# Optimization experiments

Hardware: AMD Instinct MI355X
Metric: run time of the kernel (lower is better)

## Reference

```python
import jax, jax.numpy as jnp
import numpy as np

B, T, D, R = 16, 4096, 512, 256

def setup_inputs() -> dict:
    key = jax.random.key(0)
    z = jax.random.normal(key, (B, T, D), dtype=jnp.float32)
    # init values from the module: gegenbauer_weights = [3,0,0], temporal_alpha = -10.0
    gegenbauer_weights = jnp.array([3.0, 0.0, 0.0], dtype=jnp.float32)
    temporal_alpha = jnp.array(-10.0, dtype=jnp.float32)
    # uniformly spaced landmarks, truncated to int like torch.linspace(...).long()
    landmarks = jnp.asarray(np.linspace(0, T - 1, R).astype(np.int64))
    return {"z": z, "gegenbauer_weights": gegenbauer_weights, "temporal_alpha": temporal_alpha, "landmarks": landmarks}

def reference(z, gegenbauer_weights, temporal_alpha, landmarks):
    Bz, Tz, d = z.shape
    # F.normalize(z, dim=-1) with eps=1e-12
    norm = jnp.linalg.norm(z, axis=-1, keepdims=True)
    Q = z / jnp.maximum(norm, 1e-12)
    K = Q[:, landmarks, :]                                   # [B, R, d]
    C = jnp.einsum('btd,brd->btr', Q, K)                     # [B, T, R]
    positions = jnp.arange(Tz)[:, None]                      # [T, 1]
    lm = landmarks[None, :]                                  # [1, R]
    causal_mask = (lm < positions).astype(z.dtype)           # [T, R]
    C_masked = C * causal_mask[None, :, :]
    # Gegenbauer mixture
    alpha = jax.nn.softmax(gegenbauer_weights)
    P1 = (1.0 + C_masked) * 0.5
    P2 = (3.0 * C_masked * C_masked - 1.0) * 0.5
    P3 = (5.0 * C_masked * C_masked * C_masked - 3.0 * C_masked) * 0.5
    Phi = alpha[0] * P1 + alpha[1] * P2 + alpha[2] * P3
    # temporal decay
    temporal_dist = jnp.clip((positions.astype(z.dtype) - lm.astype(z.dtype)) / Tz, 0.0, None)  # [T, R]
    alpha_td = jax.nn.softplus(temporal_alpha)
    Phi = Phi * jnp.exp(-alpha_td * temporal_dist)[None, :, :]
    # rowsum normalize
    row_sum = jnp.maximum(Phi.sum(axis=-1, keepdims=True), 1e-6)
    Phi = Phi / row_sum
    # append constant-1 basis column
    ones = jnp.ones((Bz, Tz, 1), dtype=z.dtype)
    return jnp.concatenate([Phi, ones], axis=-1)             # [B, T, R+1]
```

## Files before the change

kernel.cpp:

```cpp
#include <hip/hip_runtime.h>


typedef float f32x4 __attribute__((ext_vector_type(4)));
typedef short s16x8 __attribute__((ext_vector_type(8)));
typedef unsigned short u16x4 __attribute__((ext_vector_type(4)));
typedef unsigned short u16x8 __attribute__((ext_vector_type(8)));

__device__ __forceinline__ unsigned short f2bf(float f) {
    unsigned u = __builtin_bit_cast(unsigned, f);
    return (unsigned short)((u + 0x7FFFu + ((u >> 16) & 1u)) >> 16);
}

__device__ __forceinline__ int load_lm(const void* lms_raw, int idx) {
    const int* l32 = (const int*)lms_raw;
    if (l32[1] == 0) {
        const long long* l64 = (const long long*)lms_raw;
        return (int)l64[idx];
    }
    return l32[idx];
}

__device__ __forceinline__ void scalars(const float* gw, const float* ta,
                                        float& a0, float& a1, float& a2, float& atd) {
    float w0 = gw[0], w1 = gw[1], w2 = gw[2];
    float wm = fmaxf(w0, fmaxf(w1, w2));
    float e0 = __expf(w0 - wm), e1 = __expf(w1 - wm), e2 = __expf(w2 - wm);
    float einv = 1.0f / (e0 + e1 + e2);
    a0 = e0 * einv; a1 = e1 * einv; a2 = e2 * einv;
    float tv = ta[0];
    atd = (tv > 0.0f) ? (tv + log1pf(__expf(-tv))) : log1pf(__expf(tv));
}

__global__ void build_kt(const float* __restrict__ z,
                         const void* __restrict__ lms_raw,
                         unsigned char* __restrict__ kb) {
    const int b = blockIdx.x >> 8;
    const int r = blockIdx.x & 255;
    const int L = threadIdx.x;
    const int lm = load_lm(lms_raw, r);

    const f32x4* zrow = (const f32x4*)(z + ((size_t)b * 4096 + (size_t)lm) * 512);
    f32x4 v0 = zrow[L * 2 + 0];
    f32x4 v1 = zrow[L * 2 + 1];
    float ss = v0.x*v0.x + v0.y*v0.y + v0.z*v0.z + v0.w*v0.w
             + v1.x*v1.x + v1.y*v1.y + v1.z*v1.z + v1.w*v1.w;
    #pragma unroll
    for (int off = 32; off >= 1; off >>= 1) ss += __shfl_xor(ss, off, 64);
    float inv = 1.0f / fmaxf(sqrtf(ss), 1e-12f);

    u16x8 o;
    o[0]=f2bf(v0.x*inv); o[1]=f2bf(v0.y*inv); o[2]=f2bf(v0.z*inv); o[3]=f2bf(v0.w*inv);
    o[4]=f2bf(v1.x*inv); o[5]=f2bf(v1.y*inv); o[6]=f2bf(v1.z*inv); o[7]=f2bf(v1.w*inv);

    const int rt = r >> 4;
    const int c  = r & 15;
    const int ks = L >> 2;
    const int g  = L & 3;
    size_t off = (size_t)b * 262144
               + (size_t)(ks * 16 + rt) * 1024 + (size_t)(c * 4 + g) * 16;
    *(u16x8*)(kb + off) = o;
}

#define LDB(S, KS) do { \
    B##S##0 = *(const u16x8*)(kbw + (size_t)((KS) * 16 + rt0 + 0) * 1024); \
    B##S##1 = *(const u16x8*)(kbw + (size_t)((KS) * 16 + rt0 + 1) * 1024); \
} while (0)

#define LDA(AV, KK) do { \
    AV##0 = *(const s16x8*)(qtile + ((KK) * 2 + 0) * 1024 + aoff); \
    AV##1 = *(const s16x8*)(qtile + ((KK) * 2 + 1) * 1024 + aoff); \
} while (0)

#define MM(AV, S) do { \
    s16x8 ba_ = __builtin_bit_cast(s16x8, B##S##0); \
    s16x8 bb_ = __builtin_bit_cast(s16x8, B##S##1); \
    acc00 = __builtin_amdgcn_mfma_f32_16x16x32_bf16(AV##0, ba_, acc00, 0, 0, 0); \
    acc01 = __builtin_amdgcn_mfma_f32_16x16x32_bf16(AV##0, bb_, acc01, 0, 0, 0); \
    acc10 = __builtin_amdgcn_mfma_f32_16x16x32_bf16(AV##1, ba_, acc10, 0, 0, 0); \
    acc11 = __builtin_amdgcn_mfma_f32_16x16x32_bf16(AV##1, bb_, acc11, 0, 0, 0); \
} while (0)

#define STEP(KS, AC, AN, S) do { \
    if ((KS) + 1 < 16) LDA(AN, (KS) + 1); \
    MM(AC, S); \
    if ((KS) + 4 < 16) LDB(S, (KS) + 4); \
} while (0)

__global__ __launch_bounds__(512, 6) void nystrom_mfma(const float* __restrict__ z,
                                                       const float* __restrict__ gw,
                                                       const float* __restrict__ ta,
                                                       const void* __restrict__ lms_raw,
                                                       const unsigned char* __restrict__ kb,
                                                       float* __restrict__ out) {
    __shared__ unsigned char qtile[32 * 1024];
    __shared__ float s_invn[32];
    __shared__ float s_rs[8][32];
    __shared__ float s_rsi[32];

    const int tid  = threadIdx.x;
    const int lane = tid & 63;
    const int w    = tid >> 6;

    const int wgid = (blockIdx.x & 7) * 256 + (blockIdx.x >> 3);
    const int b    = wgid >> 7;
    const int t0   = (wgid & 127) * 32;

    const int c = lane & 15;
    const int g = lane >> 4;
    const int aoff = (c * 4 + g) * 16;

    float sa0, sa1, sa2, alpha_td;
    scalars(gw, ta, sa0, sa1, sa2, alpha_td);
    const float C0 = 0.5f * (sa0 - sa1);

    const unsigned char* kbw = kb + (size_t)b * 262144 + (size_t)(c * 4 + g) * 16;
    const int rt0 = 2 * w;

    u16x8 B00, B01, B10, B11, B20, B21, B30, B31;
    LDB(0, 0); LDB(1, 1); LDB(2, 2); LDB(3, 3);

    const int lmv0 = load_lm(lms_raw, 32 * w + c);
    const int lmv1 = load_lm(lms_raw, 32 * w + 16 + c);
    const float elm0 = __expf(alpha_td * (float)lmv0 * (1.0f / 4096.0f));
    const float elm1 = __expf(alpha_td * (float)lmv1 * (1.0f / 4096.0f));

    {
        const int row = tid >> 4, part = tid & 15;
        const f32x4* zr = (const f32x4*)(z + ((size_t)b * 4096 + (size_t)(t0 + row)) * 512);
        f32x4 v[8];
        #pragma unroll
        for (int i = 0; i < 8; ++i) v[i] = zr[part + 16 * i];
        const int base = (row >> 4) * 1024 + ((row & 15) * 4 + ((part >> 1) & 3)) * 16
                       + (part & 1) * 8 + (part >> 3) * 2048;
        float ss = 0.0f;
        #pragma unroll
        for (int i = 0; i < 8; ++i) {
            f32x4 vv = v[i];
            ss += vv.x*vv.x + vv.y*vv.y + vv.z*vv.z + vv.w*vv.w;
            u16x4 hh; hh[0]=f2bf(vv.x); hh[1]=f2bf(vv.y); hh[2]=f2bf(vv.z); hh[3]=f2bf(vv.w);
            *(u16x4*)(qtile + base + i * 4096) = hh;
        }
        ss += __shfl_xor(ss, 1, 64);
        ss += __shfl_xor(ss, 2, 64);
        ss += __shfl_xor(ss, 4, 64);
        ss += __shfl_xor(ss, 8, 64);
        if (part == 0) s_invn[row] = 1.0f / fmaxf(sqrtf(ss), 1e-12f);
    }
    __syncthreads();

    f32x4 acc00 = {0,0,0,0}, acc01 = {0,0,0,0};
    f32x4 acc10 = {0,0,0,0}, acc11 = {0,0,0,0};

    s16x8 A00, A01, A10, A11;
    LDA(A0, 0);

    STEP( 0, A0, A1, 0);  STEP( 1, A1, A0, 1);
    STEP( 2, A0, A1, 2);  STEP( 3, A1, A0, 3);
    STEP( 4, A0, A1, 0);  STEP( 5, A1, A0, 1);
    STEP( 6, A0, A1, 2);  STEP( 7, A1, A0, 3);
    STEP( 8, A0, A1, 0);  STEP( 9, A1, A0, 1);
    STEP(10, A0, A1, 2);  STEP(11, A1, A0, 3);
    STEP(12, A0, A1, 0);  STEP(13, A1, A0, 1);
    STEP(14, A0, A1, 2);  STEP(15, A1, A0, 3);

    f32x4 acc[2][2] = {{acc00, acc01}, {acc10, acc11}};
    const int   lmv[2] = {lmv0, lmv1};
    const float elm[2] = {elm0, elm1};

    float eA[2], eB[4];
    #pragma unroll
    for (int tf = 0; tf < 2; ++tf)
        eA[tf] = __expf(-alpha_td * (float)(t0 + tf * 16) * (1.0f / 4096.0f));
    #pragma unroll
    for (int q = 0; q < 4; ++q)
        eB[q] = __expf(-alpha_td * (float)(g * 4 + q) * (1.0f / 4096.0f));
    float invn[2][4];
    #pragma unroll
    for (int tf = 0; tf < 2; ++tf)
        #pragma unroll
        for (int q = 0; q < 4; ++q)
            invn[tf][q] = s_invn[tf * 16 + g * 4 + q];

    float phi[2][2][4];
    float rsum[2][4];
    #pragma unroll
    for (int tf = 0; tf < 2; ++tf) {
        #pragma unroll
        for (int q = 0; q < 4; ++q) {
            int tg = t0 + tf * 16 + g * 4 + q;
            float et = eA[tf] * eB[q];
            float s = 0.0f;
            #pragma unroll
            for (int nf = 0; nf < 2; ++nf) {
                float v = acc[tf][nf][q] * invn[tf][q];
                float p;
                if (lmv[nf] < tg) {
                    float c2 = v * v;
                    float p1 = fmaf(0.5f, v, 0.5f);
                    float p2 = fmaf(1.5f, c2, -0.5f);
                    float p3 = v * fmaf(2.5f, c2, -1.5f);
                    p = (sa0 * p1 + sa1 * p2 + sa2 * p3) * (et * elm[nf]);
                } else {
                    p = C0;
                }
                phi[tf][nf][q] = p;
                s += p;
            }
            rsum[tf][q] = s;
        }
    }

    #pragma unroll
    for (int tf = 0; tf < 2; ++tf)
        #pragma unroll
        for (int q = 0; q < 4; ++q) {
            float s = rsum[tf][q];
            s += __shfl_xor(s, 1, 64);
            s += __shfl_xor(s, 2, 64);
            s += __shfl_xor(s, 4, 64);
            s += __shfl_xor(s, 8, 64);
            rsum[tf][q] = s;
        }
    if (c == 0) {
        #pragma unroll
        for (int tf = 0; tf < 2; ++tf)
            #pragma unroll
            for (int q = 0; q < 4; ++q)
                s_rs[w][tf * 16 + g * 4 + q] = rsum[tf][q];
    }
    __syncthreads();
    if (tid < 32) {
        float s = 0.0f;
        #pragma unroll
        for (int i = 0; i < 8; ++i) s += s_rs[i][tid];
        s_rsi[tid] = 1.0f / fmaxf(s, 1e-6f);
    }
    __syncthreads();

    #pragma unroll
    for (int tf = 0; tf < 2; ++tf)
        #pragma unroll
        for (int q = 0; q < 4; ++q) {
            int tl = tf * 16 + g * 4 + q;
            float ri = s_rsi[tl];
            size_t obase = ((size_t)b * 4096 + (size_t)(t0 + tl)) * 257
                         + (size_t)(32 * w + c);
            #pragma unroll
            for (int nf = 0; nf < 2; ++nf)
                out[obase + nf * 16] = phi[tf][nf][q] * ri;
        }
    if (tid < 32)
        out[((size_t)b * 4096 + (size_t)(t0 + tid)) * 257 + 256] = 1.0f;
}

extern "C" void kernel_launch(void* const* d_in, const int* in_sizes, int n_in,
                              void* d_out, int out_size, void* d_ws, size_t ws_size,
                              hipStream_t stream) {
    const float* z   = (const float*)d_in[0];
    const float* gw  = (const float*)d_in[1];
    const float* ta  = (const float*)d_in[2];
    const void*  lms = (const void*)d_in[3];
    float* out = (float*)d_out;
    unsigned char* kb = (unsigned char*)d_ws;

    build_kt<<<16 * 256, 64, 0, stream>>>(z, lms, kb);
    nystrom_mfma<<<2048, 512, 0, stream>>>(z, gw, ta, lms, kb, out);
}
```

Before: 66.46 us.

## Precompute bf16 Q in MFMA-packed layout in separate prep kernel

Adds a prep kernel that converts z to bf16 in the MFMA operand layout and stores per-row inverse norms in workspace. The main kernel then streams A operands straight from global memory with a 4-deep register prefetch instead of staging them in LDS behind a barrier. This removes the LDS tile and the __syncthreads from the main kernel, but adds an extra full pass over z plus a write and re-read of the bf16 copy. The occupancy hint in the launch bounds also drops from 6 to 4.

```diff
diff --git a/kernel.cpp b/kernel.cpp
--- a/kernel.cpp
+++ b/kernel.cpp
@@ -3,7 +3,6 @@
 
 typedef float f32x4 __attribute__((ext_vector_type(4)));
 typedef short s16x8 __attribute__((ext_vector_type(8)));
-typedef unsigned short u16x4 __attribute__((ext_vector_type(4)));
 typedef unsigned short u16x8 __attribute__((ext_vector_type(8)));
 
 __device__ __forceinline__ unsigned short f2bf(float f) {
@@ -31,6 +30,31 @@
     atd = (tv > 0.0f) ? (tv + log1pf(__expf(-tv))) : log1pf(__expf(tv));
 }
 
+__global__ __launch_bounds__(256) void prep_q(const float* __restrict__ z,
+                                              unsigned char* __restrict__ qp,
+                                              float* __restrict__ invn) {
+    const int gw   = blockIdx.x * 4 + (threadIdx.x >> 6);
+    const int lane = threadIdx.x & 63;
+
+    const f32x4* zr = (const f32x4*)(z + (size_t)gw * 512);
+    f32x4 v0 = zr[lane * 2 + 0];
+    f32x4 v1 = zr[lane * 2 + 1];
+    float ss = v0.x*v0.x + v0.y*v0.y + v0.z*v0.z + v0.w*v0.w
+             + v1.x*v1.x + v1.y*v1.y + v1.z*v1.z + v1.w*v1.w;
+    #pragma unroll
+    for (int off = 32; off >= 1; off >>= 1) ss += __shfl_xor(ss, off, 64);
+    if (lane == 0) invn[gw] = 1.0f / fmaxf(sqrtf(ss), 1e-12f);
+
+    u16x8 o;
+    o[0]=f2bf(v0.x); o[1]=f2bf(v0.y); o[2]=f2bf(v0.z); o[3]=f2bf(v0.w);
+    o[4]=f2bf(v1.x); o[5]=f2bf(v1.y); o[6]=f2bf(v1.z); o[7]=f2bf(v1.w);
+
+    size_t addr = (size_t)(gw >> 5) * 32768
+                + (size_t)(((lane >> 2) * 2 + ((gw >> 4) & 1)) * 1024)
+                + (size_t)((((lane & 3) * 16 + (gw & 15)) * 16));
+    *(u16x8*)(qp + addr) = o;
+}
+
 __global__ void build_kt(const float* __restrict__ z,
                          const void* __restrict__ lms_raw,
                          unsigned char* __restrict__ kb) {
@@ -66,34 +90,32 @@
     B##S##1 = *(const u16x8*)(kbw + (size_t)((KS) * 16 + rt0 + 1) * 1024); \
 } while (0)
 
-#define LDA(AV, KK) do { \
-    AV##0 = *(const s16x8*)(qtile + ((KK) * 2 + 0) * 1024 + aoff); \
-    AV##1 = *(const s16x8*)(qtile + ((KK) * 2 + 1) * 1024 + aoff); \
-} while (0)
-
-#define MM(AV, S) do { \
+#define LDA(S, KS) do { \
+    A##S##0 = *(const s16x8*)(qpb + ((KS) * 2 + 0) * 1024); \
+    A##S##1 = *(const s16x8*)(qpb + ((KS) * 2 + 1) * 1024); \
+} while (0)
+
+#define MM(S) do { \
     s16x8 ba_ = __builtin_bit_cast(s16x8, B##S##0); \
     s16x8 bb_ = __builtin_bit_cast(s16x8, B##S##1); \
-    acc00 = __builtin_amdgcn_mfma_f32_16x16x32_bf16(AV##0, ba_, acc00, 0, 0, 0); \
-    acc01 = __builtin_amdgcn_mfma_f32_16x16x32_bf16(AV##0, bb_, acc01, 0, 0, 0); \
-    acc10 = __builtin_amdgcn_mfma_f32_16x16x32_bf16(AV##1, ba_, acc10, 0, 0, 0); \
-    acc11 = __builtin_amdgcn_mfma_f32_16x16x32_bf16(AV##1, bb_, acc11, 0, 0, 0); \
-} while (0)
-
-#define STEP(KS, AC, AN, S) do { \
-    if ((KS) + 1 < 16) LDA(AN, (KS) + 1); \
-    MM(AC, S); \
-    if ((KS) + 4 < 16) LDB(S, (KS) + 4); \
-} while (0)
-
-__global__ __launch_bounds__(512, 6) void nystrom_mfma(const float* __restrict__ z,
-                                                       const float* __restrict__ gw,
+    acc00 = __builtin_amdgcn_mfma_f32_16x16x32_bf16(A##S##0, ba_, acc00, 0, 0, 0); \
+    acc01 = __builtin_amdgcn_mfma_f32_16x16x32_bf16(A##S##0, bb_, acc01, 0, 0, 0); \
+    acc10 = __builtin_amdgcn_mfma_f32_16x16x32_bf16(A##S##1, ba_, acc10, 0, 0, 0); \
+    acc11 = __builtin_amdgcn_mfma_f32_16x16x32_bf16(A##S##1, bb_, acc11, 0, 0, 0); \
+} while (0)
+
+#define STEP(KS, S) do { \
+    MM(S); \
+    if ((KS) + 4 < 16) { LDA(S, (KS) + 4); LDB(S, (KS) + 4); } \
+} while (0)
+
+__global__ __launch_bounds__(512, 4) void nystrom_mfma(const float* __restrict__ gw,
                                                        const float* __restrict__ ta,
                                                        const void* __restrict__ lms_raw,
+                                                       const unsigned char* __restrict__ qp,
                                                        const unsigned char* __restrict__ kb,
+                                                       const float* __restrict__ invng,
                                                        float* __restrict__ out) {
-    __shared__ unsigned char qtile[32 * 1024];
-    __shared__ float s_invn[32];
     __shared__ float s_rs[8][32];
     __shared__ float s_rsi[32];
 
@@ -103,65 +125,39 @@
 
     const int wgid = (blockIdx.x & 7) * 256 + (blockIdx.x >> 3);
     const int b    = wgid >> 7;
-    const int t0   = (wgid & 127) * 32;
+    const int tt   = wgid & 127;
+    const int t0   = tt * 32;
 
     const int c = lane & 15;
     const int g = lane >> 4;
-    const int aoff = (c * 4 + g) * 16;
 
     float sa0, sa1, sa2, alpha_td;
     scalars(gw, ta, sa0, sa1, sa2, alpha_td);
     const float C0 = 0.5f * (sa0 - sa1);
 
+    const unsigned char* qpb = qp + (size_t)(b * 128 + tt) * 32768 + (size_t)lane * 16;
     const unsigned char* kbw = kb + (size_t)b * 262144 + (size_t)(c * 4 + g) * 16;
     const int rt0 = 2 * w;
 
     u16x8 B00, B01, B10, B11, B20, B21, B30, B31;
-    LDB(0, 0); LDB(1, 1); LDB(2, 2); LDB(3, 3);
+    s16x8 A00, A01, A10, A11, A20, A21, A30, A31;
+    LDA(0, 0); LDB(0, 0);
+    LDA(1, 1); LDB(1, 1);
+    LDA(2, 2); LDB(2, 2);
+    LDA(3, 3); LDB(3, 3);
 
     const int lmv0 = load_lm(lms_raw, 32 * w + c);
     const int lmv1 = load_lm(lms_raw, 32 * w + 16 + c);
     const float elm0 = __expf(alpha_td * (float)lmv0 * (1.0f / 4096.0f));
     const float elm1 = __expf(alpha_td * (float)lmv1 * (1.0f / 4096.0f));
 
-    {
-        const int row = tid >> 4, part = tid & 15;
-        const f32x4* zr = (const f32x4*)(z + ((size_t)b * 4096 + (size_t)(t0 + row)) * 512);
-        f32x4 v[8];
-        #pragma unroll
-        for (int i = 0; i < 8; ++i) v[i] = zr[part + 16 * i];
-        const int base = (row >> 4) * 1024 + ((row & 15) * 4 + ((part >> 1) & 3)) * 16
-                       + (part & 1) * 8 + (part >> 3) * 2048;
-        float ss = 0.0f;
-        #pragma unroll
-        for (int i = 0; i < 8; ++i) {
-            f32x4 vv = v[i];
-            ss += vv.x*vv.x + vv.y*vv.y + vv.z*vv.z + vv.w*vv.w;
-            u16x4 hh; hh[0]=f2bf(vv.x); hh[1]=f2bf(vv.y); hh[2]=f2bf(vv.z); hh[3]=f2bf(vv.w);
-            *(u16x4*)(qtile + base + i * 4096) = hh;
-        }
-        ss += __shfl_xor(ss, 1, 64);
-        ss += __shfl_xor(ss, 2, 64);
-        ss += __shfl_xor(ss, 4, 64);
-        ss += __shfl_xor(ss, 8, 64);
-        if (part == 0) s_invn[row] = 1.0f / fmaxf(sqrtf(ss), 1e-12f);
-    }
-    __syncthreads();
-
     f32x4 acc00 = {0,0,0,0}, acc01 = {0,0,0,0};
     f32x4 acc10 = {0,0,0,0}, acc11 = {0,0,0,0};
 
-    s16x8 A00, A01, A10, A11;
-    LDA(A0, 0);
-
-    STEP( 0, A0, A1, 0);  STEP( 1, A1, A0, 1);
-    STEP( 2, A0, A1, 2);  STEP( 3, A1, A0, 3);
-    STEP( 4, A0, A1, 0);  STEP( 5, A1, A0, 1);
-    STEP( 6, A0, A1, 2);  STEP( 7, A1, A0, 3);
-    STEP( 8, A0, A1, 0);  STEP( 9, A1, A0, 1);
-    STEP(10, A0, A1, 2);  STEP(11, A1, A0, 3);
-    STEP(12, A0, A1, 0);  STEP(13, A1, A0, 1);
-    STEP(14, A0, A1, 2);  STEP(15, A1, A0, 3);
+    STEP( 0, 0);  STEP( 1, 1);  STEP( 2, 2);  STEP( 3, 3);
+    STEP( 4, 0);  STEP( 5, 1);  STEP( 6, 2);  STEP( 7, 3);
+    STEP( 8, 0);  STEP( 9, 1);  STEP(10, 2);  STEP(11, 3);
+    STEP(12, 0);  STEP(13, 1);  STEP(14, 2);  STEP(15, 3);
 
     f32x4 acc[2][2] = {{acc00, acc01}, {acc10, acc11}};
     const int   lmv[2] = {lmv0, lmv1};
@@ -179,7 +175,7 @@
     for (int tf = 0; tf < 2; ++tf)
         #pragma unroll
         for (int q = 0; q < 4; ++q)
-            invn[tf][q] = s_invn[tf * 16 + g * 4 + q];
+            invn[tf][q] = invng[b * 4096 + t0 + tf * 16 + g * 4 + q];
 
     float phi[2][2][4];
     float rsum[2][4];
@@ -261,8 +257,12 @@
     const float* ta  = (const float*)d_in[2];
     const void*  lms = (const void*)d_in[3];
     float* out = (float*)d_out;
-    unsigned char* kb = (unsigned char*)d_ws;
-
+
+    unsigned char* qp   = (unsigned char*)d_ws;
+    unsigned char* kb   = qp + (size_t)16 * 128 * 32 * 1024;
+    float*         invn = (float*)(kb + (size_t)16 * 262144);
+
+    prep_q<<<16384, 256, 0, stream>>>(z, qp, invn);
     build_kt<<<16 * 256, 64, 0, stream>>>(z, lms, kb);
-    nystrom_mfma<<<2048, 512, 0, stream>>>(z, gw, ta, lms, kb, out);
-}
+    nystrom_mfma<<<2048, 512, 0, stream>>>(gw, ta, lms, qp, kb, invn, out);
+}
```

After: 109.0 us. 1.64x slower.

## Make MFMA blocks persistent over four row tiles with prefetched z loads

Applied to the files above, without the earlier changes.

Each workgroup now handles 128 time steps in four 32-row iterations instead of one, and the grid shrinks from 2048 to 512 blocks. The next tile's z rows are loaded into registers while the current tile's MFMA runs, and the K fragments are reloaded after each GEMM. The LDS Q tile moves to a row-major layout with an XOR swizzle to avoid bank conflicts. The aim is to hide global-load latency and cut per-block setup, at the cost of more registers (launch bounds lowered to 4 waves) and fewer blocks to spread over the CUs.

```diff
diff --git a/kernel.cpp b/kernel.cpp
--- a/kernel.cpp
+++ b/kernel.cpp
@@ -67,8 +67,9 @@
 } while (0)
 
 #define LDA(AV, KK) do { \
-    AV##0 = *(const s16x8*)(qtile + ((KK) * 2 + 0) * 1024 + aoff); \
-    AV##1 = *(const s16x8*)(qtile + ((KK) * 2 + 1) * 1024 + aoff); \
+    int kw_ = ((KK) * 64 + g * 16) ^ swz; \
+    AV##0 = *(const s16x8*)(qtile + (c     ) * 1024 + kw_); \
+    AV##1 = *(const s16x8*)(qtile + (c + 16) * 1024 + kw_); \
 } while (0)
 
 #define MM(AV, S) do { \
@@ -86,28 +87,44 @@
     if ((KS) + 4 < 16) LDB(S, (KS) + 4); \
 } while (0)
 
-__global__ __launch_bounds__(512, 6) void nystrom_mfma(const float* __restrict__ z,
+#define LDV(J) do { \
+    const f32x4* zr_ = (const f32x4*)(z + ((size_t)b * 4096 \
+                        + (size_t)(tbase + (J) * 32 + row)) * 512); \
+    V0 = zr_[part +  0]; V1 = zr_[part + 16]; \
+    V2 = zr_[part + 32]; V3 = zr_[part + 48]; \
+    V4 = zr_[part + 64]; V5 = zr_[part + 80]; \
+    V6 = zr_[part + 96]; V7 = zr_[part + 112]; \
+} while (0)
+
+#define STV(I, VV) do { \
+    ss += VV.x*VV.x + VV.y*VV.y + VV.z*VV.z + VV.w*VV.w; \
+    u16x4 hh_; hh_[0]=f2bf(VV.x); hh_[1]=f2bf(VV.y); hh_[2]=f2bf(VV.z); hh_[3]=f2bf(VV.w); \
+    int wi_ = ((part + 16 * (I)) * 8) ^ ((row & 7) << 4); \
+    *(u16x4*)(qtile + row * 1024 + wi_) = hh_; \
+} while (0)
+
+__global__ __launch_bounds__(512, 4) void nystrom_mfma(const float* __restrict__ z,
                                                        const float* __restrict__ gw,
                                                        const float* __restrict__ ta,
                                                        const void* __restrict__ lms_raw,
                                                        const unsigned char* __restrict__ kb,
                                                        float* __restrict__ out) {
     __shared__ unsigned char qtile[32 * 1024];
-    __shared__ float s_invn[32];
+    __shared__ float s_aux[2][32];
     __shared__ float s_rs[8][32];
-    __shared__ float s_rsi[32];
 
     const int tid  = threadIdx.x;
     const int lane = tid & 63;
     const int w    = tid >> 6;
 
-    const int wgid = (blockIdx.x & 7) * 256 + (blockIdx.x >> 3);
-    const int b    = wgid >> 7;
-    const int t0   = (wgid & 127) * 32;
+    const int wgid  = (blockIdx.x & 7) * 64 + (blockIdx.x >> 3);
+    const int b     = wgid >> 5;
+    const int tbase = (wgid & 31) * 128;
 
     const int c = lane & 15;
     const int g = lane >> 4;
-    const int aoff = (c * 4 + g) * 16;
+    const int row = tid >> 4, part = tid & 15;
+    const int swz = (c & 7) << 4;
 
     float sa0, sa1, sa2, alpha_td;
     scalars(gw, ta, sa0, sa1, sa2, alpha_td);
@@ -115,142 +132,141 @@
 
     const unsigned char* kbw = kb + (size_t)b * 262144 + (size_t)(c * 4 + g) * 16;
     const int rt0 = 2 * w;
-
-    u16x8 B00, B01, B10, B11, B20, B21, B30, B31;
-    LDB(0, 0); LDB(1, 1); LDB(2, 2); LDB(3, 3);
 
     const int lmv0 = load_lm(lms_raw, 32 * w + c);
     const int lmv1 = load_lm(lms_raw, 32 * w + 16 + c);
     const float elm0 = __expf(alpha_td * (float)lmv0 * (1.0f / 4096.0f));
     const float elm1 = __expf(alpha_td * (float)lmv1 * (1.0f / 4096.0f));
-
-    {
-        const int row = tid >> 4, part = tid & 15;
-        const f32x4* zr = (const f32x4*)(z + ((size_t)b * 4096 + (size_t)(t0 + row)) * 512);
-        f32x4 v[8];
-        #pragma unroll
-        for (int i = 0; i < 8; ++i) v[i] = zr[part + 16 * i];
-        const int base = (row >> 4) * 1024 + ((row & 15) * 4 + ((part >> 1) & 3)) * 16
-                       + (part & 1) * 8 + (part >> 3) * 2048;
-        float ss = 0.0f;
-        #pragma unroll
-        for (int i = 0; i < 8; ++i) {
-            f32x4 vv = v[i];
-            ss += vv.x*vv.x + vv.y*vv.y + vv.z*vv.z + vv.w*vv.w;
-            u16x4 hh; hh[0]=f2bf(vv.x); hh[1]=f2bf(vv.y); hh[2]=f2bf(vv.z); hh[3]=f2bf(vv.w);
-            *(u16x4*)(qtile + base + i * 4096) = hh;
-        }
-        ss += __shfl_xor(ss, 1, 64);
-        ss += __shfl_xor(ss, 2, 64);
-        ss += __shfl_xor(ss, 4, 64);
-        ss += __shfl_xor(ss, 8, 64);
-        if (part == 0) s_invn[row] = 1.0f / fmaxf(sqrtf(ss), 1e-12f);
-    }
-    __syncthreads();
-
-    f32x4 acc00 = {0,0,0,0}, acc01 = {0,0,0,0};
-    f32x4 acc10 = {0,0,0,0}, acc11 = {0,0,0,0};
-
-    s16x8 A00, A01, A10, A11;
-    LDA(A0, 0);
-
-    STEP( 0, A0, A1, 0);  STEP( 1, A1, A0, 1);
-    STEP( 2, A0, A1, 2);  STEP( 3, A1, A0, 3);
-    STEP( 4, A0, A1, 0);  STEP( 5, A1, A0, 1);
-    STEP( 6, A0, A1, 2);  STEP( 7, A1, A0, 3);
-    STEP( 8, A0, A1, 0);  STEP( 9, A1, A0, 1);
-    STEP(10, A0, A1, 2);  STEP(11, A1, A0, 3);
-    STEP(12, A0, A1, 0);  STEP(13, A1, A0, 1);
-    STEP(14, A0, A1, 2);  STEP(15, A1, A0, 3);
-
-    f32x4 acc[2][2] = {{acc00, acc01}, {acc10, acc11}};
-    const int   lmv[2] = {lmv0, lmv1};
-    const float elm[2] = {elm0, elm1};
-
-    float eA[2], eB[4];
-    #pragma unroll
-    for (int tf = 0; tf < 2; ++tf)
-        eA[tf] = __expf(-alpha_td * (float)(t0 + tf * 16) * (1.0f / 4096.0f));
+    float eB[4];
     #pragma unroll
     for (int q = 0; q < 4; ++q)
         eB[q] = __expf(-alpha_td * (float)(g * 4 + q) * (1.0f / 4096.0f));
-    float invn[2][4];
-    #pragma unroll
-    for (int tf = 0; tf < 2; ++tf)
-        #pragma unroll
-        for (int q = 0; q < 4; ++q)
-            invn[tf][q] = s_invn[tf * 16 + g * 4 + q];
-
-    float phi[2][2][4];
-    float rsum[2][4];
-    #pragma unroll
-    for (int tf = 0; tf < 2; ++tf) {
-        #pragma unroll
-        for (int q = 0; q < 4; ++q) {
-            int tg = t0 + tf * 16 + g * 4 + q;
-            float et = eA[tf] * eB[q];
+    const float d16 = __expf(-alpha_td * (16.0f / 4096.0f));
+
+    f32x4 V0, V1, V2, V3, V4, V5, V6, V7;
+    u16x8 B00, B01, B10, B11, B20, B21, B30, B31;
+    LDV(0);
+    LDB(0, 0); LDB(1, 1); LDB(2, 2); LDB(3, 3);
+
+    for (int j = 0; j < 4; ++j) {
+        const int t0 = tbase + j * 32;
+
+        {
+            float ss = 0.0f;
+            STV(0, V0); STV(1, V1); STV(2, V2); STV(3, V3);
+            STV(4, V4); STV(5, V5); STV(6, V6); STV(7, V7);
+            ss += __shfl_xor(ss, 1, 64);
+            ss += __shfl_xor(ss, 2, 64);
+            ss += __shfl_xor(ss, 4, 64);
+            ss += __shfl_xor(ss, 8, 64);
+            if (part == 0) s_aux[j & 1][row] = 1.0f / fmaxf(sqrtf(ss), 1e-12f);
+        }
+        __syncthreads();
+
+        if (j < 3) LDV(j + 1);
+
+        f32x4 acc00 = {0,0,0,0}, acc01 = {0,0,0,0};
+        f32x4 acc10 = {0,0,0,0}, acc11 = {0,0,0,0};
+
+        s16x8 A00, A01, A10, A11;
+        LDA(A0, 0);
+
+        STEP( 0, A0, A1, 0);  STEP( 1, A1, A0, 1);
+        STEP( 2, A0, A1, 2);  STEP( 3, A1, A0, 3);
+        STEP( 4, A0, A1, 0);  STEP( 5, A1, A0, 1);
+        STEP( 6, A0, A1, 2);  STEP( 7, A1, A0, 3);
+        STEP( 8, A0, A1, 0);  STEP( 9, A1, A0, 1);
+        STEP(10, A0, A1, 2);  STEP(11, A1, A0, 3);
+        STEP(12, A0, A1, 0);  STEP(13, A1, A0, 1);
+        STEP(14, A0, A1, 2);  STEP(15, A1, A0, 3);
+
+        if (j < 3) { LDB(0, 0); LDB(1, 1); LDB(2, 2); LDB(3, 3); }
+
+        f32x4 acc[2][2] = {{acc00, acc01}, {acc10, acc11}};
+        const int   lmv[2] = {lmv0, lmv1};
+        const float elm[2] = {elm0, elm1};
+
+        float eA[2];
+        eA[0] = __expf(-alpha_td * (float)t0 * (1.0f / 4096.0f));
+        eA[1] = eA[0] * d16;
+        float invn[2][4];
+        #pragma unroll
+        for (int tf = 0; tf < 2; ++tf)
+            #pragma unroll
+            for (int q = 0; q < 4; ++q)
+                invn[tf][q] = s_aux[j & 1][tf * 16 + g * 4 + q];
+
+        float phi[2][2][4];
+        float rsum[2][4];
+        #pragma unroll
+        for (int tf = 0; tf < 2; ++tf) {
+            #pragma unroll
+            for (int q = 0; q < 4; ++q) {
+                int tg = t0 + tf * 16 + g * 4 + q;
+                float et = eA[tf] * eB[q];
+                float s = 0.0f;
+                #pragma unroll
+                for (int nf = 0; nf < 2; ++nf) {
+                    float v = acc[tf][nf][q] * invn[tf][q];
+                    float p;
+                    if (lmv[nf] < tg) {
+                        float c2 = v * v;
+                        float p1 = fmaf(0.5f, v, 0.5f);
+                        float p2 = fmaf(1.5f, c2, -0.5f);
+                        float p3 = v * fmaf(2.5f, c2, -1.5f);
+                        p = (sa0 * p1 + sa1 * p2 + sa2 * p3) * (et * elm[nf]);
+                    } else {
+                        p = C0;
+                    }
+                    phi[tf][nf][q] = p;
+                    s += p;
+                }
+                rsum[tf][q] = s;
+            }
+        }
+
+        #pragma unroll
+        for (int tf = 0; tf < 2; ++tf)
+            #pragma unroll
+            for (int q = 0; q < 4; ++q) {
+                float s = rsum[tf][q];
+                s += __shfl_xor(s, 1, 64);
+                s += __shfl_xor(s, 2, 64);
+                s += __shfl_xor(s, 4, 64);
+                s += __shfl_xor(s, 8, 64);
+                rsum[tf][q] = s;
+            }
+        if (c == 0) {
+            #pragma unroll
+            for (int tf = 0; tf < 2; ++tf)
+                #pragma unroll
+                for (int q = 0; q < 4; ++q)
+                    s_rs[w][tf * 16 + g * 4 + q] = rsum[tf][q];
+        }
+        __syncthreads();
+        if (tid < 32) {
             float s = 0.0f;
             #pragma unroll
-            for (int nf = 0; nf < 2; ++nf) {
-                float v = acc[tf][nf][q] * invn[tf][q];
-                float p;
-                if (lmv[nf] < tg) {
-                    float c2 = v * v;
-                    float p1 = fmaf(0.5f, v, 0.5f);
-                    float p2 = fmaf(1.5f, c2, -0.5f);
-                    float p3 = v * fmaf(2.5f, c2, -1.5f);
-                    p = (sa0 * p1 + sa1 * p2 + sa2 * p3) * (et * elm[nf]);
-                } else {
-                    p = C0;
-                }
-                phi[tf][nf][q] = p;
-                s += p;
+            for (int i = 0; i < 8; ++i) s += s_rs[i][tid];
+            s_aux[j & 1][tid] = 1.0f / fmaxf(s, 1e-6f);
+        }
+        __syncthreads();
+
+        #pragma unroll
+        for (int tf = 0; tf < 2; ++tf)
+            #pragma unroll
+            for (int q = 0; q < 4; ++q) {
+                int tl = tf * 16 + g * 4 + q;
+                float ri = s_aux[j & 1][tl];
+                size_t obase = ((size_t)b * 4096 + (size_t)(t0 + tl)) * 257
+                             + (size_t)(32 * w + c);
+                #pragma unroll
+                for (int nf = 0; nf < 2; ++nf)
+                    out[obase + nf * 16] = phi[tf][nf][q] * ri;
             }
-            rsum[tf][q] = s;
-        }
+        if (tid < 32)
+            out[((size_t)b * 4096 + (size_t)(t0 + tid)) * 257 + 256] = 1.0f;
     }
-
-    #pragma unroll
-    for (int tf = 0; tf < 2; ++tf)
-        #pragma unroll
-        for (int q = 0; q < 4; ++q) {
-            float s = rsum[tf][q];
-            s += __shfl_xor(s, 1, 64);
-            s += __shfl_xor(s, 2, 64);
-            s += __shfl_xor(s, 4, 64);
-            s += __shfl_xor(s, 8, 64);
-            rsum[tf][q] = s;
-        }
-    if (c == 0) {
-        #pragma unroll
-        for (int tf = 0; tf < 2; ++tf)
-            #pragma unroll
-            for (int q = 0; q < 4; ++q)
-                s_rs[w][tf * 16 + g * 4 + q] = rsum[tf][q];
-    }
-    __syncthreads();
-    if (tid < 32) {
-        float s = 0.0f;
-        #pragma unroll
-        for (int i = 0; i < 8; ++i) s += s_rs[i][tid];
-        s_rsi[tid] = 1.0f / fmaxf(s, 1e-6f);
-    }
-    __syncthreads();
-
-    #pragma unroll
-    for (int tf = 0; tf < 2; ++tf)
-        #pragma unroll
-        for (int q = 0; q < 4; ++q) {
-            int tl = tf * 16 + g * 4 + q;
-            float ri = s_rsi[tl];
-            size_t obase = ((size_t)b * 4096 + (size_t)(t0 + tl)) * 257
-                         + (size_t)(32 * w + c);
-            #pragma unroll
-            for (int nf = 0; nf < 2; ++nf)
-                out[obase + nf * 16] = phi[tf][nf][q] * ri;
-        }
-    if (tid < 32)
-        out[((size_t)b * 4096 + (size_t)(t0 + tid)) * 257 + 256] = 1.0f;
 }
 
 extern "C" void kernel_launch(void* const* d_in, const int* in_sizes, int n_in,
@@ -264,5 +280,5 @@
     unsigned char* kb = (unsigned char*)d_ws;
 
     build_kt<<<16 * 256, 64, 0, stream>>>(z, lms, kb);
-    nystrom_mfma<<<2048, 512, 0, stream>>>(z, gw, ta, lms, kb, out);
-}
+    nystrom_mfma<<<512, 512, 0, stream>>>(z, gw, ta, lms, kb, out);
+}
```

After: 187.1 us. 2.81x slower.

## Make nystrom kernel persistent over 128 rows with double-buffered async Q staging

Applied to the files above, without the earlier changes.

Each workgroup now handles 128 time steps in 8 iterations of 16 rows instead of 32 rows once, launching 512 blocks instead of 2048. Each wave keeps all 16 K-tile B fragments in registers, loaded once per workgroup. Q rows are copied fp32 straight from global to LDS with global_load_lds, double-buffered so the next tile's load overlaps the current MFMA work. Row norms and the bf16 conversion (v_cvt_pk_bf16_f32) are now done inside the MFMA loop, and row sums use LDS atomics. In exchange it raises register pressure (launch bounds lowered to 4), doubles the LDS footprint through fp32 staging, and adds two barriers per iteration.

```diff
diff --git a/kernel.cpp b/kernel.cpp
--- a/kernel.cpp
+++ b/kernel.cpp
@@ -3,7 +3,6 @@
 
 typedef float f32x4 __attribute__((ext_vector_type(4)));
 typedef short s16x8 __attribute__((ext_vector_type(8)));
-typedef unsigned short u16x4 __attribute__((ext_vector_type(4)));
 typedef unsigned short u16x8 __attribute__((ext_vector_type(8)));
 
 __device__ __forceinline__ unsigned short f2bf(float f) {
@@ -31,6 +30,21 @@
     atd = (tv > 0.0f) ? (tv + log1pf(__expf(-tv))) : log1pf(__expf(tv));
 }
 
+__device__ __forceinline__ s16x8 cvt8(f32x4 a, f32x4 b) {
+    union { unsigned int u[4]; s16x8 v; } r;
+    asm("v_cvt_pk_bf16_f32 %0, %1, %2" : "=v"(r.u[0]) : "v"(a.x), "v"(a.y));
+    asm("v_cvt_pk_bf16_f32 %0, %1, %2" : "=v"(r.u[1]) : "v"(a.z), "v"(a.w));
+    asm("v_cvt_pk_bf16_f32 %0, %1, %2" : "=v"(r.u[2]) : "v"(b.x), "v"(b.y));
+    asm("v_cvt_pk_bf16_f32 %0, %1, %2" : "=v"(r.u[3]) : "v"(b.z), "v"(b.w));
+    return r.v;
+}
+
+__device__ __forceinline__ void gl16(const float* g, unsigned char* l) {
+    __builtin_amdgcn_global_load_lds(
+        (const __attribute__((address_space(1))) unsigned int*)g,
+        (__attribute__((address_space(3))) unsigned int*)l, 16, 0, 0);
+}
+
 __global__ void build_kt(const float* __restrict__ z,
                          const void* __restrict__ lms_raw,
                          unsigned char* __restrict__ kb) {
@@ -61,53 +75,54 @@
     *(u16x8*)(kb + off) = o;
 }
 
-#define LDB(S, KS) do { \
-    B##S##0 = *(const u16x8*)(kbw + (size_t)((KS) * 16 + rt0 + 0) * 1024); \
-    B##S##1 = *(const u16x8*)(kbw + (size_t)((KS) * 16 + rt0 + 1) * 1024); \
+#define FOREACH_KS(X) X(0) X(1) X(2) X(3) X(4) X(5) X(6) X(7) \
+                      X(8) X(9) X(10) X(11) X(12) X(13) X(14) X(15)
+
+#define DECLB(KS) u16x8 Bq##KS##a, Bq##KS##b;
+#define LOADB(KS) \
+    Bq##KS##a = *(const u16x8*)(kbw + (size_t)((KS) * 16 + rt0 + 0) * 1024); \
+    Bq##KS##b = *(const u16x8*)(kbw + (size_t)((KS) * 16 + rt0 + 1) * 1024);
+
+#define KSTEP(KS) { \
+    f32x4 a0_ = *(const f32x4*)(qb + (KS) * 2048); \
+    f32x4 a1_ = *(const f32x4*)(qb + (KS) * 2048 + 1024); \
+    ss = fmaf(a0_.x,a0_.x, fmaf(a0_.y,a0_.y, fmaf(a0_.z,a0_.z, fmaf(a0_.w,a0_.w, ss)))); \
+    ss = fmaf(a1_.x,a1_.x, fmaf(a1_.y,a1_.y, fmaf(a1_.z,a1_.z, fmaf(a1_.w,a1_.w, ss)))); \
+    s16x8 af_ = cvt8(a0_, a1_); \
+    acc0 = __builtin_amdgcn_mfma_f32_16x16x32_bf16(af_, __builtin_bit_cast(s16x8, Bq##KS##a), acc0, 0, 0, 0); \
+    acc1 = __builtin_amdgcn_mfma_f32_16x16x32_bf16(af_, __builtin_bit_cast(s16x8, Bq##KS##b), acc1, 0, 0, 0); \
+}
+
+#define STAGE(BUF, JT) do { \
+    const float* zs_ = z + ((size_t)b * 4096 \
+                       + (size_t)(tbase + (JT) * 16 + (lane & 15))) * 512 \
+                       + (lane >> 4) * 8; \
+    unsigned char* qd_ = &qtile[BUF][4 * w][0]; \
+    gl16(zs_ + (2 * w + 0) * 32 + 0, qd_ +    0); \
+    gl16(zs_ + (2 * w + 0) * 32 + 4, qd_ + 1024); \
+    gl16(zs_ + (2 * w + 1) * 32 + 0, qd_ + 2048); \
+    gl16(zs_ + (2 * w + 1) * 32 + 4, qd_ + 3072); \
 } while (0)
 
-#define LDA(AV, KK) do { \
-    AV##0 = *(const s16x8*)(qtile + ((KK) * 2 + 0) * 1024 + aoff); \
-    AV##1 = *(const s16x8*)(qtile + ((KK) * 2 + 1) * 1024 + aoff); \
-} while (0)
-
-#define MM(AV, S) do { \
-    s16x8 ba_ = __builtin_bit_cast(s16x8, B##S##0); \
-    s16x8 bb_ = __builtin_bit_cast(s16x8, B##S##1); \
-    acc00 = __builtin_amdgcn_mfma_f32_16x16x32_bf16(AV##0, ba_, acc00, 0, 0, 0); \
-    acc01 = __builtin_amdgcn_mfma_f32_16x16x32_bf16(AV##0, bb_, acc01, 0, 0, 0); \
-    acc10 = __builtin_amdgcn_mfma_f32_16x16x32_bf16(AV##1, ba_, acc10, 0, 0, 0); \
-    acc11 = __builtin_amdgcn_mfma_f32_16x16x32_bf16(AV##1, bb_, acc11, 0, 0, 0); \
-} while (0)
-
-#define STEP(KS, AC, AN, S) do { \
-    if ((KS) + 1 < 16) LDA(AN, (KS) + 1); \
-    MM(AC, S); \
-    if ((KS) + 4 < 16) LDB(S, (KS) + 4); \
-} while (0)
-
-__global__ __launch_bounds__(512, 6) void nystrom_mfma(const float* __restrict__ z,
+__global__ __launch_bounds__(512, 4) void nystrom_mfma(const float* __restrict__ z,
                                                        const float* __restrict__ gw,
                                                        const float* __restrict__ ta,
                                                        const void* __restrict__ lms_raw,
                                                        const unsigned char* __restrict__ kb,
                                                        float* __restrict__ out) {
-    __shared__ unsigned char qtile[32 * 1024];
-    __shared__ float s_invn[32];
-    __shared__ float s_rs[8][32];
-    __shared__ float s_rsi[32];
+    __shared__ unsigned char qtile[2][32][1024];
+    __shared__ float s_rs[2][16];
 
     const int tid  = threadIdx.x;
     const int lane = tid & 63;
     const int w    = tid >> 6;
 
-    const int wgid = (blockIdx.x & 7) * 256 + (blockIdx.x >> 3);
-    const int b    = wgid >> 7;
-    const int t0   = (wgid & 127) * 32;
+    const int wgid  = (blockIdx.x & 7) * 64 + (blockIdx.x >> 3);
+    const int b     = wgid >> 5;
+    const int tbase = (wgid & 31) * 128;
 
     const int c = lane & 15;
     const int g = lane >> 4;
-    const int aoff = (c * 4 + g) * 16;
 
     float sa0, sa1, sa2, alpha_td;
     scalars(gw, ta, sa0, sa1, sa2, alpha_td);
@@ -116,141 +131,95 @@
     const unsigned char* kbw = kb + (size_t)b * 262144 + (size_t)(c * 4 + g) * 16;
     const int rt0 = 2 * w;
 
-    u16x8 B00, B01, B10, B11, B20, B21, B30, B31;
-    LDB(0, 0); LDB(1, 1); LDB(2, 2); LDB(3, 3);
+    FOREACH_KS(DECLB)
+    FOREACH_KS(LOADB)
 
     const int lmv0 = load_lm(lms_raw, 32 * w + c);
     const int lmv1 = load_lm(lms_raw, 32 * w + 16 + c);
     const float elm0 = __expf(alpha_td * (float)lmv0 * (1.0f / 4096.0f));
     const float elm1 = __expf(alpha_td * (float)lmv1 * (1.0f / 4096.0f));
-
-    {
-        const int row = tid >> 4, part = tid & 15;
-        const f32x4* zr = (const f32x4*)(z + ((size_t)b * 4096 + (size_t)(t0 + row)) * 512);
-        f32x4 v[8];
-        #pragma unroll
-        for (int i = 0; i < 8; ++i) v[i] = zr[part + 16 * i];
-        const int base = (row >> 4) * 1024 + ((row & 15) * 4 + ((part >> 1) & 3)) * 16
-                       + (part & 1) * 8 + (part >> 3) * 2048;
-        float ss = 0.0f;
-        #pragma unroll
-        for (int i = 0; i < 8; ++i) {
-            f32x4 vv = v[i];
-            ss += vv.x*vv.x + vv.y*vv.y + vv.z*vv.z + vv.w*vv.w;
-            u16x4 hh; hh[0]=f2bf(vv.x); hh[1]=f2bf(vv.y); hh[2]=f2bf(vv.z); hh[3]=f2bf(vv.w);
-            *(u16x4*)(qtile + base + i * 4096) = hh;
-        }
-        ss += __shfl_xor(ss, 1, 64);
-        ss += __shfl_xor(ss, 2, 64);
-        ss += __shfl_xor(ss, 4, 64);
-        ss += __shfl_xor(ss, 8, 64);
-        if (part == 0) s_invn[row] = 1.0f / fmaxf(sqrtf(ss), 1e-12f);
-    }
-    __syncthreads();
-
-    f32x4 acc00 = {0,0,0,0}, acc01 = {0,0,0,0};
-    f32x4 acc10 = {0,0,0,0}, acc11 = {0,0,0,0};
-
-    s16x8 A00, A01, A10, A11;
-    LDA(A0, 0);
-
-    STEP( 0, A0, A1, 0);  STEP( 1, A1, A0, 1);
-    STEP( 2, A0, A1, 2);  STEP( 3, A1, A0, 3);
-    STEP( 4, A0, A1, 0);  STEP( 5, A1, A0, 1);
-    STEP( 6, A0, A1, 2);  STEP( 7, A1, A0, 3);
-    STEP( 8, A0, A1, 0);  STEP( 9, A1, A0, 1);
-    STEP(10, A0, A1, 2);  STEP(11, A1, A0, 3);
-    STEP(12, A0, A1, 0);  STEP(13, A1, A0, 1);
-    STEP(14, A0, A1, 2);  STEP(15, A1, A0, 3);
-
-    f32x4 acc[2][2] = {{acc00, acc01}, {acc10, acc11}};
-    const int   lmv[2] = {lmv0, lmv1};
-    const float elm[2] = {elm0, elm1};
-
-    float eA[2], eB[4];
-    #pragma unroll
-    for (int tf = 0; tf < 2; ++tf)
-        eA[tf] = __expf(-alpha_td * (float)(t0 + tf * 16) * (1.0f / 4096.0f));
+    float eR[4];
     #pragma unroll
     for (int q = 0; q < 4; ++q)
-        eB[q] = __expf(-alpha_td * (float)(g * 4 + q) * (1.0f / 4096.0f));
-    float invn[2][4];
-    #pragma unroll
-    for (int tf = 0; tf < 2; ++tf)
-        #pragma unroll
-        for (int q = 0; q < 4; ++q)
-            invn[tf][q] = s_invn[tf * 16 + g * 4 + q];
-
-    float phi[2][2][4];
-    float rsum[2][4];
-    #pragma unroll
-    for (int tf = 0; tf < 2; ++tf) {
+        eR[q] = __expf(-alpha_td * (float)(g * 4 + q) * (1.0f / 4096.0f));
+
+    if (tid < 32) s_rs[tid >> 4][tid & 15] = 0.0f;
+
+    STAGE(0, 0);
+
+    #pragma unroll 1
+    for (int j = 0; j < 8; ++j) {
+        if (j < 7) STAGE((j + 1) & 1, j + 1);
+
+        asm volatile("s_waitcnt vmcnt(4) lgkmcnt(0)" ::: "memory");
+        __builtin_amdgcn_sched_barrier(0);
+        __builtin_amdgcn_s_barrier();
+
+        const unsigned char* qb = &qtile[j & 1][0][0] + lane * 16;
+        f32x4 acc0 = {0, 0, 0, 0}, acc1 = {0, 0, 0, 0};
+        float ss = 0.0f;
+
+        FOREACH_KS(KSTEP)
+
+        ss += __shfl_xor(ss, 16, 64);
+        ss += __shfl_xor(ss, 32, 64);
+
+        const int t0 = tbase + j * 16;
+        const float eAj = __expf(-alpha_td * (float)t0 * (1.0f / 4096.0f));
+
+        float phi0[4], phi1[4], rsum[4];
         #pragma unroll
         for (int q = 0; q < 4; ++q) {
-            int tg = t0 + tf * 16 + g * 4 + q;
-            float et = eA[tf] * eB[q];
-            float s = 0.0f;
-            #pragma unroll
-            for (int nf = 0; nf < 2; ++nf) {
-                float v = acc[tf][nf][q] * invn[tf][q];
-                float p;
-                if (lmv[nf] < tg) {
-                    float c2 = v * v;
-                    float p1 = fmaf(0.5f, v, 0.5f);
-                    float p2 = fmaf(1.5f, c2, -0.5f);
-                    float p3 = v * fmaf(2.5f, c2, -1.5f);
-                    p = (sa0 * p1 + sa1 * p2 + sa2 * p3) * (et * elm[nf]);
-                } else {
-                    p = C0;
-                }
-                phi[tf][nf][q] = p;
-                s += p;
-            }
-            rsum[tf][q] = s;
-        }
-    }
-
-    #pragma unroll
-    for (int tf = 0; tf < 2; ++tf)
-        #pragma unroll
-        for (int q = 0; q < 4; ++q) {
-            float s = rsum[tf][q];
+            int drow = g * 4 + q;
+            float ssq = __shfl(ss, drow, 64);
+            float invn = 1.0f / fmaxf(sqrtf(ssq), 1e-12f);
+            int tg = t0 + drow;
+            float et = eAj * eR[q];
+            float v0 = acc0[q] * invn;
+            float v1 = acc1[q] * invn;
+            float p0, p1;
+            if (lmv0 < tg) {
+                float c2 = v0 * v0;
+                p0 = (sa0 * fmaf(0.5f, v0, 0.5f) + sa1 * fmaf(1.5f, c2, -0.5f)
+                    + sa2 * (v0 * fmaf(2.5f, c2, -1.5f))) * (et * elm0);
+            } else p0 = C0;
+            if (lmv1 < tg) {
+                float c2 = v1 * v1;
+                p1 = (sa0 * fmaf(0.5f, v1, 0.5f) + sa1 * fmaf(1.5f, c2, -0.5f)
+                    + sa2 * (v1 * fmaf(2.5f, c2, -1.5f))) * (et * elm1);
+            } else p1 = C0;
+            phi0[q] = p0; phi1[q] = p1;
+            float s = p0 + p1;
             s += __shfl_xor(s, 1, 64);
             s += __shfl_xor(s, 2, 64);
             s += __shfl_xor(s, 4, 64);
             s += __shfl_xor(s, 8, 64);
-            rsum[tf][q] = s;
+            rsum[q] = s;
         }
-    if (c == 0) {
-        #pragma unroll
-        for (int tf = 0; tf < 2; ++tf)
+        if (c == 0) {
             #pragma unroll
             for (int q = 0; q < 4; ++q)
-                s_rs[w][tf * 16 + g * 4 + q] = rsum[tf][q];
-    }
-    __syncthreads();
-    if (tid < 32) {
-        float s = 0.0f;
-        #pragma unroll
-        for (int i = 0; i < 8; ++i) s += s_rs[i][tid];
-        s_rsi[tid] = 1.0f / fmaxf(s, 1e-6f);
-    }
-    __syncthreads();
-
-    #pragma unroll
-    for (int tf = 0; tf < 2; ++tf)
+                atomicAdd(&s_rs[j & 1][g * 4 + q], rsum[q]);
+        }
+
+        asm volatile("s_waitcnt lgkmcnt(0)" ::: "memory");
+        __builtin_amdgcn_sched_barrier(0);
+        __builtin_amdgcn_s_barrier();
+
         #pragma unroll
         for (int q = 0; q < 4; ++q) {
-            int tl = tf * 16 + g * 4 + q;
-            float ri = s_rsi[tl];
-            size_t obase = ((size_t)b * 4096 + (size_t)(t0 + tl)) * 257
+            int drow = g * 4 + q;
+            float ri = 1.0f / fmaxf(s_rs[j & 1][drow], 1e-6f);
+            size_t obase = ((size_t)b * 4096 + (size_t)(t0 + drow)) * 257
                          + (size_t)(32 * w + c);
-            #pragma unroll
-            for (int nf = 0; nf < 2; ++nf)
-                out[obase + nf * 16] = phi[tf][nf][q] * ri;
+            out[obase]      = phi0[q] * ri;
+            out[obase + 16] = phi1[q] * ri;
         }
-    if (tid < 32)
-        out[((size_t)b * 4096 + (size_t)(t0 + tid)) * 257 + 256] = 1.0f;
+        if (tid < 16)
+            out[((size_t)b * 4096 + (size_t)(t0 + tid)) * 257 + 256] = 1.0f;
+
+        if (tid < 16) s_rs[(j & 1) ^ 1][tid] = 0.0f;
+    }
 }
 
 extern "C" void kernel_launch(void* const* d_in, const int* in_sizes, int n_in,
@@ -264,5 +233,5 @@
     unsigned char* kb = (unsigned char*)d_ws;
 
     build_kt<<<16 * 256, 64, 0, stream>>>(z, lms, kb);
-    nystrom_mfma<<<2048, 512, 0, stream>>>(z, gw, ta, lms, kb, out);
-}
+    nystrom_mfma<<<512, 512, 0, stream>>>(z, gw, ta, lms, kb, out);
+}
```

Result: slower. 136.3 us (+105.1%).
